# Optimization experiments

Hardware: AMD Instinct MI355X
Metric: run time of the kernel (lower is better)

Reference implementation:

```python
import jax, jax.numpy as jnp
import numpy as np

B, N, D = 4, 4096, 1024
DFF = 4 * D
K = 2048  # max(1, int(N * 0.5))


def setup_inputs() -> dict:
    key = jax.random.key(0)
    ks = jax.random.split(key, 4)
    x = jax.random.normal(ks[0], (B, N, D), dtype=jnp.float32)
    gate_w = jax.random.normal(ks[1], (1, D), dtype=jnp.float32) * 0.02
    w1 = jax.random.normal(ks[2], (D, DFF), dtype=jnp.float32) * (1.0 / np.sqrt(D))
    b1 = jnp.zeros((DFF,), dtype=jnp.float32)
    w2 = jax.random.normal(ks[3], (DFF, D), dtype=jnp.float32) * (1.0 / np.sqrt(DFF))
    b2 = jnp.zeros((D,), dtype=jnp.float32)
    return {"x": x, "gate_w": gate_w, "w1": w1, "b1": b1, "w2": w2, "b2": b2, "k": K}


def reference(x, gate_w, w1, b1, w2, b2, k):
    # scores: [B, N] = gate(x).squeeze(-1)
    scores = jnp.einsum("bnd,d->bn", x, gate_w[0])
    _, topk = jax.lax.top_k(scores, k)          # [B, k] token indices
    # gather selected tokens: [B, k, D]
    x_sel = jnp.take_along_axis(x, topk[:, :, None], axis=1)
    # ffn (d -> 4d -> d, GELU) + residual on selected tokens only
    h = jax.nn.gelu(x_sel @ w1 + b1) @ w2 + b2
    x_proc = x_sel + h
    # scatter processed tokens back into a copy of x
    b_idx = jnp.arange(x.shape[0])[:, None]      # [B, 1]
    out = x.at[b_idx, topk].set(x_proc)
    return out
```

## Files before the change

### kernel.cpp

```cpp
#include <hip/hip_runtime.h>
#include <math.h>

#define B_   4
#define N_   4096
#define D_   1024
#define DFF_ 4096
#define K_   2048

typedef __attribute__((ext_vector_type(8))) short short8;
typedef __attribute__((ext_vector_type(4))) float float4v;

__device__ __forceinline__ unsigned short f2bf(float f) {
    unsigned int u = __float_as_uint(f);
    u = (u + 0x7fffu + ((u >> 16) & 1u)) >> 16;
    return (unsigned short)u;
}

__device__ __forceinline__ void gld16(const void* g, void* l) {
    __builtin_amdgcn_global_load_lds((const __attribute__((address_space(1))) void*)g,
                                     (__attribute__((address_space(3))) void*)l, 16, 0, 0);
}

__global__ __launch_bounds__(256) void clear_flags_kernel(int* __restrict__ flags) {
    flags[blockIdx.x * 256 + threadIdx.x] = 0;
}

__global__ __launch_bounds__(256) void scores_kernel(const float* __restrict__ x,
                                                     const float* __restrict__ gate_w,
                                                     float* __restrict__ scores) {
    int wave = (blockIdx.x * blockDim.x + threadIdx.x) >> 6;
    int lane = threadIdx.x & 63;
    if (wave >= B_ * N_) return;
    const float4* xr = (const float4*)(x + (size_t)wave * D_);
    const float4* g  = (const float4*)gate_w;
    float acc = 0.f;
    #pragma unroll
    for (int j = 0; j < D_ / 4 / 64; ++j) {
        float4 a = xr[lane + j * 64];
        float4 b = g[lane + j * 64];
        acc += a.x * b.x + a.y * b.y + a.z * b.z + a.w * b.w;
    }
    #pragma unroll
    for (int off = 32; off > 0; off >>= 1) acc += __shfl_down(acc, off, 64);
    if (lane == 0) scores[wave] = acc;
}

__global__ __launch_bounds__(1024) void select_topk_kernel(const float* __restrict__ scores,
                                                           int* __restrict__ topk,
                                                           int* __restrict__ flags) {
    __shared__ unsigned key[N_];
    __shared__ unsigned hist[256];
    __shared__ unsigned rev[256];
    __shared__ int      cnt[1024];
    __shared__ int      sh_bin, sh_rem, sh_ngt;
    int b = blockIdx.x, tid = threadIdx.x;

    for (int i = tid; i < N_; i += 1024) {
        unsigned u = __float_as_uint(scores[b * N_ + i]);
        key[i] = (u & 0x80000000u) ? ~u : (u | 0x80000000u);
    }
    if (tid == 0) sh_ngt = 0;
    __syncthreads();

    unsigned prefix = 0, pmask = 0;
    int rem = K_;
    for (int shift = 24; shift >= 0; shift -= 8) {
        if (tid < 256) hist[tid] = 0;
        __syncthreads();
        for (int i = tid; i < N_; i += 1024) {
            unsigned k = key[i];
            if ((k & pmask) == prefix) atomicAdd(&hist[(k >> shift) & 255u], 1u);
        }
        __syncthreads();
        if (tid < 256) rev[tid] = hist[255 - tid];
        __syncthreads();
        #pragma unroll
        for (int off = 1; off < 256; off <<= 1) {
            unsigned v = 0, a = 0;
            if (tid < 256) { v = rev[tid]; a = (tid >= off) ? rev[tid - off] : 0u; }
            __syncthreads();
            if (tid < 256) rev[tid] = v + a;
            __syncthreads();
        }
        if (tid < 256) {
            unsigned mysuf = rev[255 - tid];
            unsigned nxt   = (tid == 255) ? 0u : rev[254 - tid];
            if ((int)mysuf >= rem && (int)nxt < rem) { sh_bin = tid; sh_rem = rem - (int)nxt; }
        }
        __syncthreads();
        prefix |= ((unsigned)sh_bin) << shift;
        pmask  |= 0xffu << shift;
        rem = sh_rem;
        __syncthreads();
    }
    unsigned T = prefix;
    int c_gt = K_ - rem;

    for (int i = tid; i < N_; i += 1024) {
        if (key[i] > T) {
            int pos = atomicAdd(&sh_ngt, 1);
            topk[b * K_ + pos] = i;
            flags[b * N_ + i] = 1;
        }
    }
    int base = tid * 4, c = 0;
    #pragma unroll
    for (int j = 0; j < 4; ++j) c += (key[base + j] == T);
    cnt[tid] = c;
    __syncthreads();
    #pragma unroll
    for (int off = 1; off < 1024; off <<= 1) {
        int v = cnt[tid];
        int a = (tid >= off) ? cnt[tid - off] : 0;
        __syncthreads();
        cnt[tid] = v + a;
        __syncthreads();
    }
    int r = cnt[tid] - c;
    #pragma unroll
    for (int j = 0; j < 4; ++j) {
        if (key[base + j] == T) {
            if (r < rem) { topk[b * K_ + c_gt + r] = base + j; flags[b * N_ + base + j] = 1; }
            ++r;
        }
    }
}

__global__ __launch_bounds__(256) void copy_unsel_kernel(const float* __restrict__ x,
                                                         const int* __restrict__ flags,
                                                         float* __restrict__ out) {
    int row = blockIdx.x;
    if (flags[row]) return;
    const float4* src = (const float4*)(x + (size_t)row * D_);
    float4*       dst = (float4*)(out + (size_t)row * D_);
    dst[threadIdx.x] = src[threadIdx.x];
}

__global__ __launch_bounds__(256) void gather_convert_kernel(const float* __restrict__ x,
                                                             const int* __restrict__ topk,
                                                             unsigned short* __restrict__ xsel) {
    int r = blockIdx.x;
    int t = threadIdx.x;
    int gb = r >> 11;
    int tok = topk[r];
    const float4* src = (const float4*)(x + ((size_t)(gb * N_ + tok)) * D_);
    float4 v = src[t];
    ushort4 o;
    o.x = f2bf(v.x); o.y = f2bf(v.y); o.z = f2bf(v.z); o.w = f2bf(v.w);
    ((ushort4*)(xsel + (size_t)r * D_))[t] = o;
}

__global__ __launch_bounds__(256) void transpose_convert_kernel(const float* __restrict__ src,
                                                                unsigned short* __restrict__ dst,
                                                                int R, int C) {
    __shared__ float tile[32][33];
    int tx = threadIdx.x, ty = threadIdx.y;
    int c = blockIdx.x * 32 + tx;
    int r0 = blockIdx.y * 32;
    #pragma unroll
    for (int j = ty; j < 32; j += 8) tile[j][tx] = src[(size_t)(r0 + j) * C + c];
    __syncthreads();
    int dc = blockIdx.y * 32 + tx;
    int dr0 = blockIdx.x * 32;
    #pragma unroll
    for (int j = ty; j < 32; j += 8) dst[(size_t)(dr0 + j) * R + dc] = f2bf(tile[tx][j]);
}

__global__ __launch_bounds__(256) void ffn1_mfma_kernel(const unsigned short* __restrict__ A,
                                                        const unsigned short* __restrict__ Bt,
                                                        const float* __restrict__ b1,
                                                        unsigned short* __restrict__ h1) {
    constexpr int K = D_;
    __shared__ __align__(16) unsigned short As[128 * 32];
    __shared__ __align__(16) unsigned short Bs[128 * 32];
    int t = threadIdx.x;
    int w = t >> 6, lane = t & 63;
    int quad = lane >> 4, lr = lane & 15;
    int wm = w >> 1, wn = w & 1;
    int row0 = blockIdx.x * 128, col0 = blockIdx.y * 128;

    const char* ga0 = (const char*)(A + (size_t)(row0 + (t >> 2)) * K) + (t & 3) * 16;
    const char* ga1 = ga0 + (size_t)64 * K * 2;
    const char* gb0 = (const char*)(Bt + (size_t)(col0 + (t >> 2)) * K) + (t & 3) * 16;
    const char* gb1 = gb0 + (size_t)64 * K * 2;
    unsigned short* la0 = As + t * 8;   unsigned short* la1 = As + 2048 + t * 8;
    unsigned short* lb0 = Bs + t * 8;   unsigned short* lb1 = Bs + 2048 + t * 8;

    float4v acc[4][4] = {};
    for (int k0 = 0; k0 < K; k0 += 32) {
        gld16(ga0, la0); gld16(ga1, la1);
        gld16(gb0, lb0); gld16(gb1, lb1);
        ga0 += 64; ga1 += 64; gb0 += 64; gb1 += 64;
        __syncthreads();
        short8 af[4], bfv[4];
        #pragma unroll
        for (int mi = 0; mi < 4; ++mi)
            af[mi] = *(const short8*)(As + (size_t)(wm * 64 + mi * 16 + lr) * 32 + quad * 8);
        #pragma unroll
        for (int ni = 0; ni < 4; ++ni)
            bfv[ni] = *(const short8*)(Bs + (size_t)(wn * 64 + ni * 16 + lr) * 32 + quad * 8);
        #pragma unroll
        for (int mi = 0; mi < 4; ++mi)
            #pragma unroll
            for (int ni = 0; ni < 4; ++ni)
                acc[mi][ni] = __builtin_amdgcn_mfma_f32_16x16x32_bf16(af[mi], bfv[ni], acc[mi][ni], 0, 0, 0);
        __syncthreads();
    }

    #pragma unroll
    for (int ni = 0; ni < 4; ++ni) {
        int col = col0 + wn * 64 + ni * 16 + lr;
        float bias = b1[col];
        #pragma unroll
        for (int mi = 0; mi < 4; ++mi) {
            int row = row0 + wm * 64 + mi * 16 + quad * 4;
            #pragma unroll
            for (int r = 0; r < 4; ++r) {
                float u = acc[mi][ni][r] + bias;
                float tt = 1.5957691216057308f * u * (1.0f + 0.044715f * u * u);
                float g = u / (1.0f + __expf(-tt));
                h1[(size_t)(row + r) * DFF_ + col] = f2bf(g);
            }
        }
    }
}

__global__ __launch_bounds__(256) void ffn2_mfma_kernel(const unsigned short* __restrict__ A,
                                                        const unsigned short* __restrict__ Bt,
                                                        const float* __restrict__ b2,
                                                        const float* __restrict__ x,
                                                        const int* __restrict__ topk,
                                                        float* __restrict__ out) {
    constexpr int K = DFF_;
    __shared__ __align__(16) unsigned short As[128 * 32];
    __shared__ __align__(16) unsigned short Bs[128 * 32];
    int t = threadIdx.x;
    int w = t >> 6, lane = t & 63;
    int quad = lane >> 4, lr = lane & 15;
    int wm = w >> 1, wn = w & 1;
    int row0 = blockIdx.x * 128, col0 = blockIdx.y * 128;

    const char* ga0 = (const char*)(A + (size_t)(row0 + (t >> 2)) * K) + (t & 3) * 16;
    const char* ga1 = ga0 + (size_t)64 * K * 2;
    const char* gb0 = (const char*)(Bt + (size_t)(col0 + (t >> 2)) * K) + (t & 3) * 16;
    const char* gb1 = gb0 + (size_t)64 * K * 2;
    unsigned short* la0 = As + t * 8;   unsigned short* la1 = As + 2048 + t * 8;
    unsigned short* lb0 = Bs + t * 8;   unsigned short* lb1 = Bs + 2048 + t * 8;

    float4v acc[4][4] = {};
    for (int k0 = 0; k0 < K; k0 += 32) {
        gld16(ga0, la0); gld16(ga1, la1);
        gld16(gb0, lb0); gld16(gb1, lb1);
        ga0 += 64; ga1 += 64; gb0 += 64; gb1 += 64;
        __syncthreads();
        short8 af[4], bfv[4];
        #pragma unroll
        for (int mi = 0; mi < 4; ++mi)
            af[mi] = *(const short8*)(As + (size_t)(wm * 64 + mi * 16 + lr) * 32 + quad * 8);
        #pragma unroll
        for (int ni = 0; ni < 4; ++ni)
            bfv[ni] = *(const short8*)(Bs + (size_t)(wn * 64 + ni * 16 + lr) * 32 + quad * 8);
        #pragma unroll
        for (int mi = 0; mi < 4; ++mi)
            #pragma unroll
            for (int ni = 0; ni < 4; ++ni)
                acc[mi][ni] = __builtin_amdgcn_mfma_f32_16x16x32_bf16(af[mi], bfv[ni], acc[mi][ni], 0, 0, 0);
        __syncthreads();
    }

    #pragma unroll
    for (int mi = 0; mi < 4; ++mi) {
        #pragma unroll
        for (int r = 0; r < 4; ++r) {
            int row = row0 + wm * 64 + mi * 16 + quad * 4 + r;
            int gb = row >> 11;
            int tok = topk[row];
            size_t base = ((size_t)(gb * N_ + tok)) * D_;
            #pragma unroll
            for (int ni = 0; ni < 4; ++ni) {
                int col = col0 + wn * 64 + ni * 16 + lr;
                out[base + col] = x[base + col] + acc[mi][ni][r] + b2[col];
            }
        }
    }
}

extern "C" void kernel_launch(void* const* d_in, const int* in_sizes, int n_in,
                              void* d_out, int out_size, void* d_ws, size_t ws_size,
                              hipStream_t stream) {
    const float* x      = (const float*)d_in[0];
    const float* gate_w = (const float*)d_in[1];
    const float* w1     = (const float*)d_in[2];
    const float* b1     = (const float*)d_in[3];
    const float* w2     = (const float*)d_in[4];
    const float* b2     = (const float*)d_in[5];
    float* out = (float*)d_out;

    char* ws = (char*)d_ws;
    float*          scores = (float*)ws;
    int*            topk   = (int*)(ws + (64 << 10));
    int*            flags  = (int*)(ws + (96 << 10));
    unsigned short* xsel   = (unsigned short*)(ws + (160 << 10));
    unsigned short* w1t    = (unsigned short*)(ws + (160 << 10) + (16 << 20));
    unsigned short* w2t    = (unsigned short*)(ws + (160 << 10) + (24 << 20));
    unsigned short* h1     = (unsigned short*)(ws + (160 << 10) + (32 << 20));

    clear_flags_kernel<<<B_ * N_ / 256, 256, 0, stream>>>(flags);
    scores_kernel<<<(B_ * N_) / 4, 256, 0, stream>>>(x, gate_w, scores);
    select_topk_kernel<<<B_, 1024, 0, stream>>>(scores, topk, flags);

    transpose_convert_kernel<<<dim3(DFF_ / 32, D_ / 32), dim3(32, 8), 0, stream>>>(w1, w1t, D_, DFF_);
    transpose_convert_kernel<<<dim3(D_ / 32, DFF_ / 32), dim3(32, 8), 0, stream>>>(w2, w2t, DFF_, D_);

    gather_convert_kernel<<<B_ * K_, 256, 0, stream>>>(x, topk, xsel);
    copy_unsel_kernel<<<B_ * N_, 256, 0, stream>>>(x, flags, out);

    ffn1_mfma_kernel<<<dim3(64, 32), 256, 0, stream>>>(xsel, w1t, b1, h1);
    ffn2_mfma_kernel<<<dim3(64, 8), 256, 0, stream>>>(h1, w2t, b2, x, topk, out);
}
```

Baseline: 368.5 us.

## Fuse preprocessing kernels, speed up top-k scans, and stage FFN1 epilogue through LDS

```diff
diff --git a/kernel.cpp b/kernel.cpp
--- a/kernel.cpp
+++ b/kernel.cpp
@@ -21,16 +21,14 @@
                                      (__attribute__((address_space(3))) void*)l, 16, 0, 0);
 }
 
-__global__ __launch_bounds__(256) void clear_flags_kernel(int* __restrict__ flags) {
-    flags[blockIdx.x * 256 + threadIdx.x] = 0;
-}
-
 __global__ __launch_bounds__(256) void scores_kernel(const float* __restrict__ x,
                                                      const float* __restrict__ gate_w,
-                                                     float* __restrict__ scores) {
+                                                     float* __restrict__ scores,
+                                                     int* __restrict__ slot) {
     int wave = (blockIdx.x * blockDim.x + threadIdx.x) >> 6;
     int lane = threadIdx.x & 63;
     if (wave >= B_ * N_) return;
+    if (lane == 1) slot[wave] = -1;
     const float4* xr = (const float4*)(x + (size_t)wave * D_);
     const float4* g  = (const float4*)gate_w;
     float acc = 0.f;
@@ -47,13 +45,13 @@
 
 __global__ __launch_bounds__(1024) void select_topk_kernel(const float* __restrict__ scores,
                                                            int* __restrict__ topk,
-                                                           int* __restrict__ flags) {
+                                                           int* __restrict__ slot) {
     __shared__ unsigned key[N_];
     __shared__ unsigned hist[256];
-    __shared__ unsigned rev[256];
-    __shared__ int      cnt[1024];
-    __shared__ int      sh_bin, sh_rem, sh_ngt;
+    __shared__ int sh_bin, sh_rem, sh_ngt;
+    __shared__ int wsum[16], woff[16];
     int b = blockIdx.x, tid = threadIdx.x;
+    int lane = tid & 63, wid = tid >> 6;
 
     for (int i = tid; i < N_; i += 1024) {
         unsigned u = __float_as_uint(scores[b * N_ + i]);
@@ -72,96 +70,107 @@
             if ((k & pmask) == prefix) atomicAdd(&hist[(k >> shift) & 255u], 1u);
         }
         __syncthreads();
-        if (tid < 256) rev[tid] = hist[255 - tid];
-        __syncthreads();
-        #pragma unroll
-        for (int off = 1; off < 256; off <<= 1) {
-            unsigned v = 0, a = 0;
-            if (tid < 256) { v = rev[tid]; a = (tid >= off) ? rev[tid - off] : 0u; }
-            __syncthreads();
-            if (tid < 256) rev[tid] = v + a;
-            __syncthreads();
-        }
-        if (tid < 256) {
-            unsigned mysuf = rev[255 - tid];
-            unsigned nxt   = (tid == 255) ? 0u : rev[254 - tid];
-            if ((int)mysuf >= rem && (int)nxt < rem) { sh_bin = tid; sh_rem = rem - (int)nxt; }
+        if (tid < 64) {
+            unsigned v0 = hist[4 * lane], v1 = hist[4 * lane + 1];
+            unsigned v2 = hist[4 * lane + 2], v3 = hist[4 * lane + 3];
+            unsigned s3 = v3, s2 = v2 + s3, s1 = v1 + s2, s0 = v0 + s1;
+            unsigned t = s0;
+            #pragma unroll
+            for (int off = 1; off < 64; off <<= 1) {
+                unsigned u = __shfl_down(t, off, 64);
+                if (lane + off < 64) t += u;
+            }
+            unsigned above = t - s0;
+            unsigned S0 = s0 + above, S1 = s1 + above, S2 = s2 + above, S3 = s3 + above;
+            unsigned R = (unsigned)rem;
+            if (S0 >= R && S1 < R) { sh_bin = 4 * lane;     sh_rem = rem - (int)S1; }
+            if (S1 >= R && S2 < R) { sh_bin = 4 * lane + 1; sh_rem = rem - (int)S2; }
+            if (S2 >= R && S3 < R) { sh_bin = 4 * lane + 2; sh_rem = rem - (int)S3; }
+            if (S3 >= R && above < R) { sh_bin = 4 * lane + 3; sh_rem = rem - (int)above; }
         }
         __syncthreads();
         prefix |= ((unsigned)sh_bin) << shift;
         pmask  |= 0xffu << shift;
         rem = sh_rem;
-        __syncthreads();
     }
     unsigned T = prefix;
     int c_gt = K_ - rem;
 
     for (int i = tid; i < N_; i += 1024) {
-        if (key[i] > T) {
-            int pos = atomicAdd(&sh_ngt, 1);
+        bool p = key[i] > T;
+        unsigned long long m = __ballot(p);
+        int cnt = __popcll(m);
+        int basepos = 0;
+        if (lane == 0 && cnt) basepos = atomicAdd(&sh_ngt, cnt);
+        basepos = __shfl(basepos, 0, 64);
+        if (p) {
+            int pos = basepos + __popcll(m & ((1ULL << lane) - 1ULL));
             topk[b * K_ + pos] = i;
-            flags[b * N_ + i] = 1;
+            slot[b * N_ + i] = b * K_ + pos;
         }
     }
     int base = tid * 4, c = 0;
     #pragma unroll
     for (int j = 0; j < 4; ++j) c += (key[base + j] == T);
-    cnt[tid] = c;
+    int sc = c;
+    #pragma unroll
+    for (int off = 1; off < 64; off <<= 1) {
+        int u = __shfl_up(sc, off, 64);
+        if (lane >= off) sc += u;
+    }
+    if (lane == 63) wsum[wid] = sc;
     __syncthreads();
-    #pragma unroll
-    for (int off = 1; off < 1024; off <<= 1) {
-        int v = cnt[tid];
-        int a = (tid >= off) ? cnt[tid - off] : 0;
-        __syncthreads();
-        cnt[tid] = v + a;
-        __syncthreads();
-    }
-    int r = cnt[tid] - c;
+    if (tid == 0) {
+        int run = 0;
+        #pragma unroll
+        for (int j = 0; j < 16; ++j) { woff[j] = run; run += wsum[j]; }
+    }
+    __syncthreads();
+    int r = woff[wid] + sc - c;
     #pragma unroll
     for (int j = 0; j < 4; ++j) {
         if (key[base + j] == T) {
-            if (r < rem) { topk[b * K_ + c_gt + r] = base + j; flags[b * N_ + base + j] = 1; }
+            if (r < rem) {
+                topk[b * K_ + c_gt + r] = base + j;
+                slot[b * N_ + base + j] = b * K_ + c_gt + r;
+            }
             ++r;
         }
     }
 }
 
-__global__ __launch_bounds__(256) void copy_unsel_kernel(const float* __restrict__ x,
-                                                         const int* __restrict__ flags,
-                                                         float* __restrict__ out) {
+__global__ __launch_bounds__(256) void gather_copy_kernel(const float* __restrict__ x,
+                                                          const int* __restrict__ slot,
+                                                          unsigned short* __restrict__ xsel,
+                                                          float* __restrict__ out) {
     int row = blockIdx.x;
-    if (flags[row]) return;
-    const float4* src = (const float4*)(x + (size_t)row * D_);
-    float4*       dst = (float4*)(out + (size_t)row * D_);
-    dst[threadIdx.x] = src[threadIdx.x];
-}
-
-__global__ __launch_bounds__(256) void gather_convert_kernel(const float* __restrict__ x,
-                                                             const int* __restrict__ topk,
-                                                             unsigned short* __restrict__ xsel) {
-    int r = blockIdx.x;
     int t = threadIdx.x;
-    int gb = r >> 11;
-    int tok = topk[r];
-    const float4* src = (const float4*)(x + ((size_t)(gb * N_ + tok)) * D_);
-    float4 v = src[t];
-    ushort4 o;
-    o.x = f2bf(v.x); o.y = f2bf(v.y); o.z = f2bf(v.z); o.w = f2bf(v.w);
-    ((ushort4*)(xsel + (size_t)r * D_))[t] = o;
-}
-
-__global__ __launch_bounds__(256) void transpose_convert_kernel(const float* __restrict__ src,
-                                                                unsigned short* __restrict__ dst,
-                                                                int R, int C) {
+    int s = slot[row];
+    float4 v = ((const float4*)(x + (size_t)row * D_))[t];
+    if (s >= 0) {
+        ushort4 o;
+        o.x = f2bf(v.x); o.y = f2bf(v.y); o.z = f2bf(v.z); o.w = f2bf(v.w);
+        ((ushort4*)(xsel + (size_t)s * D_))[t] = o;
+    } else {
+        ((float4*)(out + (size_t)row * D_))[t] = v;
+    }
+}
+
+__global__ __launch_bounds__(256) void transpose_both_kernel(const float* __restrict__ w1,
+                                                             const float* __restrict__ w2,
+                                                             unsigned short* __restrict__ w1t,
+                                                             unsigned short* __restrict__ w2t) {
     __shared__ float tile[32][33];
-    int tx = threadIdx.x, ty = threadIdx.y;
-    int c = blockIdx.x * 32 + tx;
-    int r0 = blockIdx.y * 32;
+    int bid = blockIdx.x;
+    const float* src; unsigned short* dst; int R, C, bx, by;
+    if (bid < 4096) { src = w1; dst = w1t; R = D_;   C = DFF_; bx = bid & 127;          by = bid >> 7; }
+    else            { src = w2; dst = w2t; R = DFF_; C = D_;   bx = (bid - 4096) & 31;  by = (bid - 4096) >> 5; }
+    int tx = threadIdx.x & 31, ty = threadIdx.x >> 5;
+    int c = bx * 32 + tx, r0 = by * 32;
     #pragma unroll
     for (int j = ty; j < 32; j += 8) tile[j][tx] = src[(size_t)(r0 + j) * C + c];
     __syncthreads();
-    int dc = blockIdx.y * 32 + tx;
-    int dr0 = blockIdx.x * 32;
+    int dc = by * 32 + tx, dr0 = bx * 32;
     #pragma unroll
     for (int j = ty; j < 32; j += 8) dst[(size_t)(dr0 + j) * R + dc] = f2bf(tile[tx][j]);
 }
@@ -171,8 +180,10 @@
                                                         const float* __restrict__ b1,
                                                         unsigned short* __restrict__ h1) {
     constexpr int K = D_;
-    __shared__ __align__(16) unsigned short As[128 * 32];
-    __shared__ __align__(16) unsigned short Bs[128 * 32];
+    __shared__ __align__(16) unsigned short smem[16384];
+    unsigned short* As = smem;
+    unsigned short* Bs = smem + 4096;
+    unsigned short* Cs = smem;
     int t = threadIdx.x;
     int w = t >> 6, lane = t & 63;
     int quad = lane >> 4, lr = lane & 15;
@@ -208,19 +219,33 @@
     }
 
     #pragma unroll
-    for (int ni = 0; ni < 4; ++ni) {
-        int col = col0 + wn * 64 + ni * 16 + lr;
-        float bias = b1[col];
-        #pragma unroll
-        for (int mi = 0; mi < 4; ++mi) {
-            int row = row0 + wm * 64 + mi * 16 + quad * 4;
-            #pragma unroll
-            for (int r = 0; r < 4; ++r) {
-                float u = acc[mi][ni][r] + bias;
-                float tt = 1.5957691216057308f * u * (1.0f + 0.044715f * u * u);
-                float g = u / (1.0f + __expf(-tt));
-                h1[(size_t)(row + r) * DFF_ + col] = f2bf(g);
+    for (int half = 0; half < 2; ++half) {
+        __syncthreads();
+        #pragma unroll
+        for (int mi2 = 0; mi2 < 2; ++mi2) {
+            int mi = half * 2 + mi2;
+            #pragma unroll
+            for (int ni = 0; ni < 4; ++ni) {
+                int col = wn * 64 + ni * 16 + lr;
+                float bias = b1[col0 + col];
+                #pragma unroll
+                for (int r = 0; r < 4; ++r) {
+                    int lrow = wm * 32 + mi2 * 16 + quad * 4 + r;
+                    float u = acc[mi][ni][r] + bias;
+                    float tt = 1.5957691216057308f * u * (1.0f + 0.044715f * u * u);
+                    float g = u / (1.0f + __expf(-tt));
+                    Cs[lrow * 132 + col] = f2bf(g);
+                }
             }
+        }
+        __syncthreads();
+        #pragma unroll
+        for (int kch = 0; kch < 4; ++kch) {
+            int ch = t + kch * 256;
+            int lrow = ch >> 4;
+            int off = (ch & 15) * 8;
+            int grow = row0 + ((lrow >> 5) << 6) + half * 32 + (lrow & 31);
+            *(short8*)(h1 + (size_t)grow * DFF_ + col0 + off) = *(const short8*)(Cs + lrow * 132 + off);
         }
     }
 }
@@ -299,21 +324,18 @@
     char* ws = (char*)d_ws;
     float*          scores = (float*)ws;
     int*            topk   = (int*)(ws + (64 << 10));
-    int*            flags  = (int*)(ws + (96 << 10));
+    int*            slot   = (int*)(ws + (96 << 10));
     unsigned short* xsel   = (unsigned short*)(ws + (160 << 10));
     unsigned short* w1t    = (unsigned short*)(ws + (160 << 10) + (16 << 20));
     unsigned short* w2t    = (unsigned short*)(ws + (160 << 10) + (24 << 20));
     unsigned short* h1     = (unsigned short*)(ws + (160 << 10) + (32 << 20));
 
-    clear_flags_kernel<<<B_ * N_ / 256, 256, 0, stream>>>(flags);
-    scores_kernel<<<(B_ * N_) / 4, 256, 0, stream>>>(x, gate_w, scores);
-    select_topk_kernel<<<B_, 1024, 0, stream>>>(scores, topk, flags);
-
-    transpose_convert_kernel<<<dim3(DFF_ / 32, D_ / 32), dim3(32, 8), 0, stream>>>(w1, w1t, D_, DFF_);
-    transpose_convert_kernel<<<dim3(D_ / 32, DFF_ / 32), dim3(32, 8), 0, stream>>>(w2, w2t, DFF_, D_);
-
-    gather_convert_kernel<<<B_ * K_, 256, 0, stream>>>(x, topk, xsel);
-    copy_unsel_kernel<<<B_ * N_, 256, 0, stream>>>(x, flags, out);
+    scores_kernel<<<(B_ * N_) / 4, 256, 0, stream>>>(x, gate_w, scores, slot);
+    select_topk_kernel<<<B_, 1024, 0, stream>>>(scores, topk, slot);
+
+    transpose_both_kernel<<<8192, 256, 0, stream>>>(w1, w2, w1t, w2t);
+
+    gather_copy_kernel<<<B_ * N_, 256, 0, stream>>>(x, slot, xsel, out);
 
     ffn1_mfma_kernel<<<dim3(64, 32), 256, 0, stream>>>(xsel, w1t, b1, h1);
     ffn2_mfma_kernel<<<dim3(64, 8), 256, 0, stream>>>(h1, w2t, b2, x, topk, out);
```

New measurement: 352.1 us. -4.4%, faster.
